# Kernel tuning notes

Hardware: AMD Instinct MI355X
Metric: run time of the kernel (lower is better)

## Reference

```python
import jax, jax.numpy as jnp
import numpy as np

B, S, H, D = 2, 2048, 16, 128
HID = H * D
ROPE_BASE = 10000.0


def _rope_tables(seq_len, dim, dtype):
    inv_freq = 1.0 / (ROPE_BASE ** (jnp.arange(0, dim, 2, dtype=jnp.float32) / dim))
    t = jnp.arange(seq_len, dtype=jnp.float32)
    freqs = jnp.einsum('s,d->sd', t, inv_freq)          # [S, D/2]
    emb = jnp.concatenate([freqs, freqs], axis=-1)       # [S, D]
    return jnp.cos(emb).astype(dtype), jnp.sin(emb).astype(dtype)


def _rotate_half(x):
    x1, x2 = jnp.split(x, 2, axis=-1)
    return jnp.concatenate([-x2, x1], axis=-1)


def _apply_rope(x, cos, sin, position_ids):
    # x: [B,H,S,D]; cos/sin: [S_emb, D]; position_ids: [B,S] or [1,S]
    c = cos[position_ids][:, None, :, :]  # [B,1,S,D]
    s = sin[position_ids][:, None, :, :]
    return x * c + _rotate_half(x) * s


def setup_inputs() -> dict:
    key = jax.random.key(0)
    ks = jax.random.split(key, 9)
    hidden_states = jax.random.normal(ks[0], (B, S, HID), jnp.float32) * 0.02
    Wq = jax.random.normal(ks[1], (HID, HID), jnp.float32) * 0.02
    Wk = jax.random.normal(ks[2], (HID, HID), jnp.float32) * 0.02
    Wv = jax.random.normal(ks[3], (HID, HID), jnp.float32) * 0.02
    Wo = jax.random.normal(ks[4], (HID, HID), jnp.float32) * 0.02
    # binary mask marking summary tokens
    sum_mask = jax.random.randint(ks[5], (B, S), 0, 2).astype(jnp.float32)
    # row-stochastic-ish averaging matrix over tokens (KV compression weights)
    raw = jax.random.uniform(ks[6], (B, S, S), jnp.float32)
    sum_attn_mask = sum_mask[:, :, None] * raw / jnp.sum(raw, axis=-1, keepdims=True)
    # additive causal mask [B,1,S,S]
    causal = jnp.tril(jnp.ones((S, S), dtype=bool))
    attention_mask = jnp.where(causal, 0.0, -1e9).astype(jnp.float32)
    attention_mask = jnp.broadcast_to(attention_mask[None, None], (B, 1, S, S))
    position_ids = jnp.broadcast_to(jnp.arange(S, dtype=jnp.int32), (B, S))
    return {
        'hidden_states': hidden_states, 'sum_mask': sum_mask,
        'sum_attn_mask': sum_attn_mask, 'attention_mask': attention_mask,
        'position_ids': position_ids, 'Wq': Wq, 'Wk': Wk, 'Wv': Wv, 'Wo': Wo,
    }


def reference(hidden_states, sum_mask, sum_attn_mask, attention_mask,
              position_ids, Wq, Wk, Wv, Wo):
    dtype = hidden_states.dtype
    # projections (F.linear: x @ W^T), then [B,H,S,D]
    def proj(W):
        return (hidden_states @ W.T).reshape(B, S, H, D).transpose(0, 2, 1, 3)
    q, k, v = proj(Wq), proj(Wk), proj(Wv)

    kv_seq_len = S
    cos, sin = _rope_tables(kv_seq_len, D, dtype)
    q = _apply_rope(q, cos, sin, position_ids)

    # KV compression: weighted token averaging injected at summary positions
    k_avg = jnp.einsum('bqk,bhkd->bhqd', sum_attn_mask, k)
    v_avg = jnp.einsum('bqk,bhkd->bhqd', sum_attn_mask, v)
    no_sum = (1.0 - sum_mask)[:, None, :, None]  # [B,1,S,1]
    k = no_sum * k + k_avg
    v = no_sum * v + v_avg

    key_pos = jnp.arange(kv_seq_len, dtype=jnp.int32)[None, :]  # [1,S]
    k = _apply_rope(k, cos, sin, key_pos)

    scale = 1.0 / np.sqrt(D)
    attn = jnp.einsum('bhqd,bhkd->bhqk', q, k) * scale
    attn = attn + attention_mask
    attn = jnp.maximum(attn, jnp.finfo(attn.dtype).min)
    attn = jax.nn.softmax(attn.astype(jnp.float32), axis=-1).astype(dtype)
    out = jnp.einsum('bhqk,bhkd->bhqd', attn, v)            # [B,H,S,D]
    out = out.transpose(0, 2, 1, 3).reshape(B, S, HID)
    return out @ Wo.T
```

## Files before the change

### kernel.cpp

```cpp
#include <hip/hip_runtime.h>
#include <cstdint>
#include <cstddef>

#define B_   2
#define S_   2048
#define H_   16
#define D_   128
#define HID_ 2048

typedef __bf16 bf16;
typedef unsigned short u16;
typedef bf16 bf16x4 __attribute__((ext_vector_type(4)));
typedef bf16 bf16x8 __attribute__((ext_vector_type(8)));
typedef u16  u16x8  __attribute__((ext_vector_type(8)));
typedef float f32x4 __attribute__((ext_vector_type(4)));

__device__ unsigned g_work;

__device__ __forceinline__ f32x4 mfma16(bf16x8 a, bf16x8 b, f32x4 c){
  return __builtin_amdgcn_mfma_f32_16x16x32_bf16(a, b, c, 0, 0, 0);
}

__device__ __forceinline__ void gload_lds16(const void* g, void* l){
  __builtin_amdgcn_global_load_lds((const __attribute__((address_space(1))) void*)g,
                                   (__attribute__((address_space(3))) void*)l, 16, 0, 0);
}

__device__ __forceinline__ void bar_lgkm(){
  asm volatile("s_waitcnt lgkmcnt(0)" ::: "memory");
  __builtin_amdgcn_s_barrier();
}
__device__ __forceinline__ void bar_full(){
  asm volatile("s_waitcnt vmcnt(0) lgkmcnt(0)" ::: "memory");
  __builtin_amdgcn_s_barrier();
}

__global__ void k_tables(float* __restrict__ cosT, float* __restrict__ sinT){
  if (blockIdx.x == 0 && threadIdx.x == 0) g_work = 0u;
  int id = blockIdx.x*256 + threadIdx.x;
  int p = id >> 6, i = id & 63;
  double f = (double)p * pow(10000.0, -(double)i/64.0);
  cosT[id] = (float)cos(f);
  sinT[id] = (float)sin(f);
}

__global__ void k_cvt_all(const float* __restrict__ a0, bf16* __restrict__ o0,
                          const float* __restrict__ a1, bf16* __restrict__ o1,
                          const float* __restrict__ w0, bf16* __restrict__ q0,
                          const float* __restrict__ w1, bf16* __restrict__ q1,
                          const float* __restrict__ w2, bf16* __restrict__ q2,
                          const float* __restrict__ w3, bf16* __restrict__ q3){
  const float* src; bf16* dst; int n4;
  switch (blockIdx.y){
    case 0: src = a0; dst = o0; n4 = 2097152; break;
    case 1: src = a1; dst = o1; n4 = 2097152; break;
    case 2: src = w0; dst = q0; n4 = 1048576; break;
    case 3: src = w1; dst = q1; n4 = 1048576; break;
    case 4: src = w2; dst = q2; n4 = 1048576; break;
    default: src = w3; dst = q3; n4 = 1048576; break;
  }
  int i = blockIdx.x*256 + threadIdx.x;
  if (i >= n4) return;
  f32x4 v = *reinterpret_cast<const f32x4*>(src + (size_t)i*4);
  bf16x4 o;
  o[0]=(bf16)v[0]; o[1]=(bf16)v[1]; o[2]=(bf16)v[2]; o[3]=(bf16)v[3];
  *reinterpret_cast<bf16x4*>(dst + (size_t)i*4) = o;
}

__global__ __launch_bounds__(256) void k_transpose_cvt(const float* __restrict__ in, bf16* __restrict__ out){
  __shared__ bf16 t[64][72];
  const int tid = threadIdx.x;
  const int b = blockIdx.z, j0 = blockIdx.x*64, s0 = blockIdx.y*64;
  #pragma unroll
  for (int u0 = 0; u0 < 4; ++u0){
    int u = u0*256 + tid;
    int r = u >> 4, c4 = (u & 15)*4;
    f32x4 v = *reinterpret_cast<const f32x4*>(in + ((size_t)b*S_ + s0 + r)*HID_ + j0 + c4);
    bf16x4 o; o[0]=(bf16)v[0]; o[1]=(bf16)v[1]; o[2]=(bf16)v[2]; o[3]=(bf16)v[3];
    *reinterpret_cast<bf16x4*>(&t[r][c4]) = o;
  }
  __syncthreads();
  #pragma unroll
  for (int u0 = 0; u0 < 4; ++u0){
    int u = u0*256 + tid;
    int r = u >> 4, c4 = (u & 15)*4;
    bf16x4 o;
    o[0] = t[c4+0][r]; o[1] = t[c4+1][r]; o[2] = t[c4+2][r]; o[3] = t[c4+3][r];
    *reinterpret_cast<bf16x4*>(out + ((size_t)b*HID_ + j0 + r)*S_ + s0 + c4) = o;
  }
}

template<int EPI>
__global__ __launch_bounds__(256) void k_gemm_nt(
    const bf16* __restrict__ A, const bf16* __restrict__ Bm, void* __restrict__ Cv,
    int Kd, size_t sAz, size_t sBz, size_t sCz, int N,
    const float* __restrict__ mask, const float* __restrict__ hid)
{
  const int tid = threadIdx.x;
  const int wid = tid >> 6, lane = tid & 63;
  const int g = lane >> 4, li = lane & 15;
  const int z = blockIdx.z;
  const int m0 = blockIdx.y*128, n0 = blockIdx.x*128;
  const int wm = wid >> 1, wn = wid & 1;
  const bf16* Ab = A + (size_t)z*sAz;
  const bf16* Bb = Bm + (size_t)z*sBz;

  __shared__ bf16 lA[128*64];
  __shared__ bf16 lB[128*64];

  f32x4 acc[4][4];
  #pragma unroll
  for (int i=0;i<4;++i)
    #pragma unroll
    for (int j=0;j<4;++j)
      acc[i][j] = {0.f,0.f,0.f,0.f};

  for (int k0 = 0; k0 < Kd; k0 += 64){
    #pragma unroll
    for (int j=0;j<4;++j){
      int ci = j*256 + tid;
      int r = ci >> 3, cb = ci & 7;
      gload_lds16(Ab + (size_t)(m0 + r)*Kd + k0 + cb*8, (char*)lA + (j*256 + wid*64)*16);
      gload_lds16(Bb + (size_t)(n0 + r)*Kd + k0 + cb*8, (char*)lB + (j*256 + wid*64)*16);
    }
    __syncthreads();
    #pragma unroll
    for (int kk=0;kk<2;++kk){
      bf16x8 af[4], bfm[4];
      #pragma unroll
      for (int i=0;i<4;++i){
        af[i]  = *reinterpret_cast<const bf16x8*>(&lA[(wm*64 + i*16 + li)*64 + kk*32 + g*8]);
        bfm[i] = *reinterpret_cast<const bf16x8*>(&lB[(wn*64 + i*16 + li)*64 + kk*32 + g*8]);
      }
      #pragma unroll
      for (int i=0;i<4;++i)
        #pragma unroll
        for (int j=0;j<4;++j)
          acc[i][j] = mfma16(af[i], bfm[j], acc[i][j]);
    }
    __syncthreads();
  }

  #pragma unroll
  for (int i=0;i<4;++i){
    #pragma unroll
    for (int j=0;j<4;++j){
      #pragma unroll
      for (int v=0;v<4;++v){
        int row = m0 + wm*64 + i*16 + g*4 + v;
        int col = n0 + wn*64 + j*16 + li;
        float x = acc[i][j][v];
        if (EPI == 1){
          x += (1.f - mask[z*S_ + row]) * hid[((size_t)z*S_ + row)*HID_ + col];
          ((bf16*)Cv)[(size_t)z*sCz + (size_t)row*N + col] = (bf16)x;
        } else if (EPI == 0){
          ((bf16*)Cv)[(size_t)row*N + col] = (bf16)x;
        } else if (EPI == 2){
          ((float*)Cv)[(size_t)row*N + col] = x;
        } else {
          if (n0 < 2048) ((bf16*)Cv)[(size_t)row*2048 + col] = (bf16)x;
          else ((bf16*)(void*)hid)[(size_t)row*2048 + col - 2048] = (bf16)x;
        }
      }
    }
  }
}

__global__ void k_rope(bf16* __restrict__ X, const float* __restrict__ cosT,
                       const float* __restrict__ sinT, const int* __restrict__ pos){
  int id = blockIdx.x*256 + threadIdx.x;
  int d4 = (id & 15)*4;
  int h  = (id >> 4) & 15;
  int s  = (id >> 8) & 2047;
  int b  = id >> 19;
  int p = pos ? pos[b*S_ + s] : s;
  size_t base = (((size_t)b*S_ + s)*H_ + h)*D_ + d4;
  f32x4 c  = *reinterpret_cast<const f32x4*>(cosT + (size_t)p*64 + d4);
  f32x4 sn = *reinterpret_cast<const f32x4*>(sinT + (size_t)p*64 + d4);
  bf16x4 x1 = *reinterpret_cast<bf16x4*>(X + base);
  bf16x4 x2 = *reinterpret_cast<bf16x4*>(X + base + 64);
  bf16x4 o1, o2;
  #pragma unroll
  for (int i=0;i<4;++i){
    float a = (float)x1[i], bb = (float)x2[i];
    o1[i] = (bf16)(a*c[i] - bb*sn[i]);
    o2[i] = (bf16)(bb*c[i] + a*sn[i]);
  }
  *reinterpret_cast<bf16x4*>(X + base) = o1;
  *reinterpret_cast<bf16x4*>(X + base + 64) = o2;
}

__global__ __launch_bounds__(256,2) void k_flash(const bf16* __restrict__ Q, const bf16* __restrict__ K,
                                                 const bf16* __restrict__ V, bf16* __restrict__ O,
                                                 float* __restrict__ OP, float* __restrict__ ML)
{
  const int tid = threadIdx.x;
  const int wid = tid >> 6, lane = tid & 63;
  const int g = lane >> 4, li = lane & 15;

  __shared__ bf16 Klds[2][64*128];
  __shared__ char VtB[128*128];
  __shared__ bf16 Plds[4][32*72];
  __shared__ int s_item;

  const int dc0 = tid & 15, kvp0 = tid >> 4;
  const int kvp1 = kvp0 + 16;

  for (;;) {
    if (tid == 0) s_item = (int)atomicAdd(&g_work, 1u);
    __syncthreads();
    const int w = s_item;
    if (w >= 672) return;

    int qx, bh, part, t0, t1;
    if (w < 96)       { qx = 10 - (w >> 5);  bh = w & 31;  part = -1; t0 = 0; t1 = 2*qx + 2; }
    else if (w < 416) { int u = w - 96;  qx = 15 - (u >> 6); int r = u & 63; bh = r >> 1; part = r & 1;
                        int nt = 2*qx + 2, mid = nt >> 1; t0 = part ? mid : 0; t1 = part ? nt : mid; }
    else              { int u = w - 416; qx = 7 - (u >> 5);  bh = u & 31;  part = -1; t0 = 0; t1 = 2*qx + 2; }

    const int qb = qx * 128;
    const size_t headoff = ((size_t)(bh >> 4)*S_*H_ + (bh & 15))*D_;
    const bf16* Kh = K + headoff;
    const u16*  Vh = (const u16*)(V + headoff);

    bf16x8 qf[2][4];
    #pragma unroll
    for (int rb=0;rb<2;++rb){
      const bf16* Qp = Q + headoff + (size_t)(qb + wid*32 + rb*16 + li)*H_*D_;
      #pragma unroll
      for (int kc=0;kc<4;++kc)
        qf[rb][kc] = *reinterpret_cast<const bf16x8*>(Qp + kc*32 + g*8);
    }

    float mrun[2][4], lrun[2][4];
    f32x4 acc[2][8];
    #pragma unroll
    for (int rb=0;rb<2;++rb){
      #pragma unroll
      for (int v=0;v<4;++v){ mrun[rb][v] = -1e30f; lrun[rb][v] = 0.f; }
      #pragma unroll
      for (int fn=0;fn<8;++fn) acc[rb][fn] = {0.f,0.f,0.f,0.f};
    }

    u16x8 vp[4];
    auto stageK = [&](int buf, int t){
      #pragma unroll
      for (int j=0;j<4;++j){
        int ci = j*256 + tid;
        int r = ci >> 4, cb = ci & 15;
        const char* src = (const char*)(Kh + (size_t)(t*64 + r)*H_*D_) + ((cb ^ (r & 7)) * 16);
        gload_lds16(src, (char*)Klds[buf] + (j*256 + wid*64)*16);
      }
    };
    auto loadV = [&](int t){
      const u16* s0p = Vh + (size_t)(t*64 + kvp0*2)*H_*D_ + dc0*8;
      const u16* s1p = Vh + (size_t)(t*64 + kvp1*2)*H_*D_ + dc0*8;
      vp[0] = *reinterpret_cast<const u16x8*>(s0p);
      vp[1] = *reinterpret_cast<const u16x8*>(s0p + H_*D_);
      vp[2] = *reinterpret_cast<const u16x8*>(s1p);
      vp[3] = *reinterpret_cast<const u16x8*>(s1p + H_*D_);
    };
    auto writeVtB = [&](){
      #pragma unroll
      for (int j=0;j<2;++j){
        int kvp = j ? kvp1 : kvp0;
        #pragma unroll
        for (int e=0;e<8;++e){
          int r = dc0*8 + e;
          int swz = (r ^ (r >> 3)) & 7;
          int addr = r*128 + (((kvp >> 2) ^ swz) << 4) + ((kvp << 2) & 12);
          *reinterpret_cast<uint32_t*>(VtB + addr) =
              (uint32_t)vp[j*2+0][e] | ((uint32_t)vp[j*2+1][e] << 16);
        }
      }
    };

    stageK(0, t0);
    loadV(t0);
    writeVtB();
    bar_full();

    int cur = 0;
    for (int t=t0; t<t1; ++t){
      const bool more = (t+1 < t1);
      if (more){ stageK(cur^1, t+1); loadV(t+1); }

      f32x4 sc[2][4];
      #pragma unroll
      for (int fc=0;fc<4;++fc){
        int r = fc*16 + li;
        bf16x8 kf[4];
        #pragma unroll
        for (int kc=0;kc<4;++kc)
          kf[kc] = *reinterpret_cast<const bf16x8*>((const char*)Klds[cur] + r*256 + (((4*kc + g) ^ (r & 7))*16));
        __builtin_amdgcn_s_setprio(1);
        #pragma unroll
        for (int rb=0;rb<2;++rb){
          f32x4 s = {0.f,0.f,0.f,0.f};
          #pragma unroll
          for (int kc=0;kc<4;++kc)
            s = mfma16(qf[rb][kc], kf[kc], s);
          sc[rb][fc] = s;
        }
        __builtin_amdgcn_s_setprio(0);
      }

      const float scale = 0.08838834764831845f;
      const int c0 = t*64;
      if (t >= 2*qx){
        #pragma unroll
        for (int rb=0;rb<2;++rb){
          const int rowg = qb + wid*32 + rb*16 + g*4;
          #pragma unroll
          for (int fc=0;fc<4;++fc){
            int col = c0 + fc*16 + li;
            #pragma unroll
            for (int v=0;v<4;++v){
              float s = sc[rb][fc][v] * scale;
              sc[rb][fc][v] = (col > rowg + v) ? -1e30f : s;
            }
          }
        }
      } else {
        #pragma unroll
        for (int rb=0;rb<2;++rb)
          #pragma unroll
          for (int fc=0;fc<4;++fc)
            #pragma unroll
            for (int v=0;v<4;++v)
              sc[rb][fc][v] *= scale;
      }

      #pragma unroll
      for (int rb=0;rb<2;++rb){
        float tm[4];
        #pragma unroll
        for (int v=0;v<4;++v){
          float m2 = fmaxf(fmaxf(sc[rb][0][v], sc[rb][1][v]), fmaxf(sc[rb][2][v], sc[rb][3][v]));
          m2 = fmaxf(m2, __shfl_xor(m2, 1));
          m2 = fmaxf(m2, __shfl_xor(m2, 2));
          m2 = fmaxf(m2, __shfl_xor(m2, 4));
          m2 = fmaxf(m2, __shfl_xor(m2, 8));
          tm[v] = m2;
        }
        bool need = false;
        #pragma unroll
        for (int v=0;v<4;++v) need = need || (tm[v] > mrun[rb][v] + 8.f);
        if (__any(need)){
          float al[4];
          #pragma unroll
          for (int v=0;v<4;++v){
            float mnew = fmaxf(mrun[rb][v], tm[v]);
            al[v] = __expf(mrun[rb][v] - mnew);
            mrun[rb][v] = mnew;
            lrun[rb][v] *= al[v];
          }
          #pragma unroll
          for (int fn=0;fn<8;++fn)
            #pragma unroll
            for (int v=0;v<4;++v) acc[rb][fn][v] *= al[v];
        }
        float rs[4] = {0.f,0.f,0.f,0.f};
        #pragma unroll
        for (int fc=0;fc<4;++fc){
          #pragma unroll
          for (int v=0;v<4;++v){
            float p = __expf(sc[rb][fc][v] - mrun[rb][v]);
            rs[v] += p;
            Plds[wid][(rb*16 + g*4 + v)*72 + fc*16 + li] = (bf16)p;
          }
        }
        #pragma unroll
        for (int v=0;v<4;++v){
          float r = rs[v];
          r += __shfl_xor(r, 1); r += __shfl_xor(r, 2);
          r += __shfl_xor(r, 4); r += __shfl_xor(r, 8);
          lrun[rb][v] += r;
        }
      }

      bf16x8 pa[2][2];
      #pragma unroll
      for (int rb=0;rb<2;++rb)
        #pragma unroll
        for (int kc=0;kc<2;++kc)
          pa[rb][kc] = *reinterpret_cast<const bf16x8*>(&Plds[wid][(rb*16 + li)*72 + kc*32 + g*8]);
      #pragma unroll
      for (int fn=0;fn<8;++fn){
        int r = fn*16 + li;
        int swz = (r ^ (r >> 3)) & 7;
        bf16x8 bv[2];
        #pragma unroll
        for (int kc=0;kc<2;++kc)
          bv[kc] = *reinterpret_cast<const bf16x8*>(VtB + r*128 + (((kc*4 + g) ^ swz) << 4));
        __builtin_amdgcn_s_setprio(1);
        #pragma unroll
        for (int rb=0;rb<2;++rb)
          #pragma unroll
          for (int kc=0;kc<2;++kc)
            acc[rb][fn] = mfma16(pa[rb][kc], bv[kc], acc[rb][fn]);
        __builtin_amdgcn_s_setprio(0);
      }

      if (more){
        bar_lgkm();
        writeVtB();
      }
      bar_full();
      cur ^= 1;
    }

    if (part < 0){
      #pragma unroll
      for (int rb=0;rb<2;++rb){
        #pragma unroll
        for (int v=0;v<4;++v){
          float inv = 1.f / lrun[rb][v];
          int row = qb + wid*32 + rb*16 + g*4 + v;
          bf16* dst = O + headoff + (size_t)row*H_*D_ + li;
          #pragma unroll
          for (int fn=0;fn<8;++fn)
            dst[fn*16] = (bf16)(acc[rb][fn][v] * inv);
        }
      }
    } else {
      const int sidx = (15 - qx)*64 + (bh << 1) + part;
      float* Od = OP + (size_t)sidx*128*128;
      #pragma unroll
      for (int rb=0;rb<2;++rb){
        #pragma unroll
        for (int v=0;v<4;++v){
          int rl = wid*32 + rb*16 + g*4 + v;
          #pragma unroll
          for (int fn=0;fn<8;++fn)
            Od[rl*128 + fn*16 + li] = acc[rb][fn][v];
          if (li == 0){
            ML[(size_t)sidx*256 + rl*2 + 0] = mrun[rb][v];
            ML[(size_t)sidx*256 + rl*2 + 1] = lrun[rb][v];
          }
        }
      }
    }
  }
}

__global__ __launch_bounds__(256) void k_merge(const float* __restrict__ OP, const float* __restrict__ ML,
                                               bf16* __restrict__ O){
  const int pair = blockIdx.x;
  const int qi = pair >> 5;
  const int qx = 15 - qi;
  const int bh = pair & 31;
  const int s0 = qi*64 + (bh << 1), s1 = s0 + 1;
  const int b = bh >> 4, h = bh & 15;
  const int qb = qx * 128;
  const int row = threadIdx.x >> 1;
  const int cseg = (threadIdx.x & 1) * 64;

  float m0 = ML[(size_t)s0*256 + row*2], l0 = ML[(size_t)s0*256 + row*2 + 1];
  float m1 = ML[(size_t)s1*256 + row*2], l1 = ML[(size_t)s1*256 + row*2 + 1];
  float m = fmaxf(m0, m1);
  float e0 = __expf(m0 - m), e1 = __expf(m1 - m);
  float inv = 1.f / (l0*e0 + l1*e1);
  const float* O0 = OP + ((size_t)s0*128 + row)*128 + cseg;
  const float* O1 = OP + ((size_t)s1*128 + row)*128 + cseg;
  bf16* dst = O + (((size_t)b*S_ + qb + row)*H_ + h)*D_ + cseg;
  #pragma unroll
  for (int c=0; c<64; c+=4){
    f32x4 a = *reinterpret_cast<const f32x4*>(O0 + c);
    f32x4 bb = *reinterpret_cast<const f32x4*>(O1 + c);
    bf16x4 o;
    #pragma unroll
    for (int i=0;i<4;++i) o[i] = (bf16)((a[i]*e0 + bb[i]*e1) * inv);
    *reinterpret_cast<bf16x4*>(dst + c) = o;
  }
}

extern "C" void kernel_launch(void* const* d_in, const int* in_sizes, int n_in,
                              void* d_out, int out_size, void* d_ws, size_t ws_size,
                              hipStream_t stream)
{
  (void)in_sizes; (void)n_in; (void)out_size; (void)ws_size;
  const float* hid   = (const float*)d_in[0];
  const float* smask = (const float*)d_in[1];
  const float* samat = (const float*)d_in[2];
  const int*   pos   = (const int*)d_in[4];
  const float* Wq = (const float*)d_in[5];
  const float* Wk = (const float*)d_in[6];
  const float* Wv = (const float*)d_in[7];
  const float* Wo = (const float*)d_in[8];
  float* out = (float*)d_out;
  char* ws = (char*)d_ws;

  const size_t SZ_TAB = (size_t)S_*64*4;
  const size_t SZ_BSH = (size_t)B_*S_*HID_*2;
  float* cosT = (float*)(ws);
  float* sinT = (float*)(ws + SZ_TAB);
  bf16* buf1 = (bf16*)(ws + 2*SZ_TAB);
  bf16* buf2 = (bf16*)(ws + 2*SZ_TAB + 1*SZ_BSH);
  bf16* buf3 = (bf16*)(ws + 2*SZ_TAB + 2*SZ_BSH);
  bf16* buf4 = (bf16*)(ws + 2*SZ_TAB + 3*SZ_BSH);
  bf16* Wqb = (bf16*)(ws + 2*SZ_TAB + 4*SZ_BSH);
  bf16* Wkb = Wqb + (size_t)HID_*HID_;
  bf16* Wvb = Wkb + (size_t)HID_*HID_;
  bf16* Wob = Wvb + (size_t)HID_*HID_;
  float* OP = (float*)Wqb;
  float* ML = OP + (size_t)320*128*128;

  k_tables<<<512,256,0,stream>>>(cosT, sinT);
  k_cvt_all<<<dim3(8192,6),256,0,stream>>>(hid, buf1, samat, buf3,
                                           Wq, Wqb, Wk, Wkb, Wv, Wvb, Wo, Wob);
  k_transpose_cvt<<<dim3(32,32,2),256,0,stream>>>(hid, buf2);

  const size_t sBat = (size_t)S_*HID_;
  k_gemm_nt<1><<<dim3(16,16,2),256,0,stream>>>(buf3, buf2, buf4, 2048, sBat, sBat, sBat, 2048, smask, hid);
  k_gemm_nt<0><<<dim3(16,32,1),256,0,stream>>>(buf1, Wqb, buf3, 2048, 0,0,0, 2048, nullptr, nullptr);
  k_rope<<<4096,256,0,stream>>>(buf3, cosT, sinT, pos);
  k_gemm_nt<3><<<dim3(32,32,1),256,0,stream>>>(buf4, Wkb, buf2, 2048, 0,0,0, 2048, nullptr, (const float*)buf1);
  k_rope<<<4096,256,0,stream>>>(buf2, cosT, sinT, nullptr);
  k_flash<<<dim3(512),256,0,stream>>>(buf3, buf2, buf1, buf4, OP, ML);
  k_merge<<<dim3(160),256,0,stream>>>(OP, ML, buf4);
  k_gemm_nt<2><<<dim3(16,32,1),256,0,stream>>>(buf4, Wob, out, 2048, 0,0,0, 2048, nullptr, nullptr);
}
```

Measured before the change: 452.2 us.

## Add 256x256-tile double-buffered GEMM with swizzled LDS for fused K/V projection

Adds a new GEMM kernel with 512 threads, 256x256 output tiles, double-buffered LDS filled by direct global-to-LDS loads, an XOR-swizzled LDS layout, and MFMA bursts raised in priority with s_setprio. Only the fused K/V projection GEMM (N=4096) uses it, replacing the 128x128-tile kernel. The aim is more reuse per LDS load, fewer bank conflicts, and overlap of the next tile's loads with the current tile's MFMAs. In exchange it uses 128KB of LDS and 128 accumulator registers per thread, which limits occupancy, and the grid shrinks to 256 blocks.

```diff
diff --git a/kernel.cpp b/kernel.cpp
--- a/kernel.cpp
+++ b/kernel.cpp
@@ -148,6 +148,135 @@
       #pragma unroll
       for (int v=0;v<4;++v){
         int row = m0 + wm*64 + i*16 + g*4 + v;
+        int col = n0 + wn*64 + j*16 + li;
+        float x = acc[i][j][v];
+        if (EPI == 1){
+          x += (1.f - mask[z*S_ + row]) * hid[((size_t)z*S_ + row)*HID_ + col];
+          ((bf16*)Cv)[(size_t)z*sCz + (size_t)row*N + col] = (bf16)x;
+        } else if (EPI == 0){
+          ((bf16*)Cv)[(size_t)row*N + col] = (bf16)x;
+        } else if (EPI == 2){
+          ((float*)Cv)[(size_t)row*N + col] = x;
+        } else {
+          if (n0 < 2048) ((bf16*)Cv)[(size_t)row*2048 + col] = (bf16)x;
+          else ((bf16*)(void*)hid)[(size_t)row*2048 + col - 2048] = (bf16)x;
+        }
+      }
+    }
+  }
+}
+
+template<int EPI>
+__global__ __launch_bounds__(512,2) void k_gemm256(
+    const bf16* __restrict__ A, const bf16* __restrict__ Bm, void* __restrict__ Cv,
+    int Kd, size_t sAz, size_t sBz, size_t sCz, int N,
+    const float* __restrict__ mask, const float* __restrict__ hid)
+{
+  const int tid = threadIdx.x;
+  const int wid = tid >> 6, lane = tid & 63;
+  const int g = lane >> 4, li = lane & 15;
+  const int wm = wid >> 2, wn = wid & 3;
+  const int z = blockIdx.z;
+  const int m0 = blockIdx.y*256, n0 = blockIdx.x*256;
+  const bf16* Ab = A + (size_t)z*sAz + (size_t)m0*Kd;
+  const bf16* Bb = Bm + (size_t)z*sBz + (size_t)n0*Kd;
+
+  __shared__ bf16 lA[2][256*64];
+  __shared__ bf16 lB[2][256*64];
+
+  const int rr0 = tid >> 3, cc = tid & 7;
+  const int rr1 = rr0 + 64;
+  const int cx0 = cc ^ (rr0 & 7);
+  const int cx1 = cc ^ (rr1 & 7);
+
+  f32x4 acc[8][4];
+  #pragma unroll
+  for (int i=0;i<8;++i)
+    #pragma unroll
+    for (int j=0;j<4;++j) acc[i][j] = {0.f,0.f,0.f,0.f};
+
+  auto stage = [&](int buf, int kt, int matsel, int half){
+    const bf16* s = matsel ? Bb : Ab;
+    char* dbase = (char*)(matsel ? lB[buf] : lA[buf]) + half*16384;
+    gload_lds16(s + (size_t)(half*128 + rr0)*Kd + kt*64 + cx0*8, dbase + (wid*64)*16);
+    gload_lds16(s + (size_t)(half*128 + rr1)*Kd + kt*64 + cx1*8, dbase + (512 + wid*64)*16);
+  };
+  auto rdA = [&](int buf, int i, int kh){
+    int row = wm*128 + i*16 + li;
+    return *reinterpret_cast<const bf16x8*>((const char*)lA[buf] + row*128 + (((kh*4 + g) ^ (row & 7))*16));
+  };
+  auto rdB = [&](int buf, int j, int kh){
+    int row = wn*64 + j*16 + li;
+    return *reinterpret_cast<const bf16x8*>((const char*)lB[buf] + row*128 + (((kh*4 + g) ^ (row & 7))*16));
+  };
+
+  const int NT = Kd >> 6;
+  stage(0,0,0,0); stage(0,0,0,1); stage(0,0,1,0); stage(0,0,1,1);
+  __syncthreads();
+
+  int cur = 0;
+  for (int kt = 0; kt < NT; ++kt){
+    const bool more = (kt+1 < NT);
+    bf16x8 af[4], bfr[4];
+
+    if (more){
+      stage(cur^1, kt+1, 0, 0); stage(cur^1, kt+1, 0, 1);
+      stage(cur^1, kt+1, 1, 0); stage(cur^1, kt+1, 1, 1);
+    }
+    #pragma unroll
+    for (int i=0;i<4;++i) af[i] = rdA(cur, i, 0);
+    #pragma unroll
+    for (int j=0;j<4;++j) bfr[j] = rdB(cur, j, 0);
+    __builtin_amdgcn_s_setprio(1);
+    #pragma unroll
+    for (int i=0;i<4;++i)
+      #pragma unroll
+      for (int j=0;j<4;++j) acc[i][j] = mfma16(af[i], bfr[j], acc[i][j]);
+    __builtin_amdgcn_s_setprio(0);
+    __builtin_amdgcn_s_barrier();
+
+    #pragma unroll
+    for (int i=0;i<4;++i) af[i] = rdA(cur, i+4, 0);
+    __builtin_amdgcn_s_setprio(1);
+    #pragma unroll
+    for (int i=0;i<4;++i)
+      #pragma unroll
+      for (int j=0;j<4;++j) acc[i+4][j] = mfma16(af[i], bfr[j], acc[i+4][j]);
+    __builtin_amdgcn_s_setprio(0);
+    __builtin_amdgcn_s_barrier();
+
+    #pragma unroll
+    for (int i=0;i<4;++i) af[i] = rdA(cur, i, 1);
+    #pragma unroll
+    for (int j=0;j<4;++j) bfr[j] = rdB(cur, j, 1);
+    __builtin_amdgcn_s_setprio(1);
+    #pragma unroll
+    for (int i=0;i<4;++i)
+      #pragma unroll
+      for (int j=0;j<4;++j) acc[i][j] = mfma16(af[i], bfr[j], acc[i][j]);
+    __builtin_amdgcn_s_setprio(0);
+    __builtin_amdgcn_s_barrier();
+
+    #pragma unroll
+    for (int i=0;i<4;++i) af[i] = rdA(cur, i+4, 1);
+    __builtin_amdgcn_s_setprio(1);
+    #pragma unroll
+    for (int i=0;i<4;++i)
+      #pragma unroll
+      for (int j=0;j<4;++j) acc[i+4][j] = mfma16(af[i], bfr[j], acc[i+4][j]);
+    __builtin_amdgcn_s_setprio(0);
+
+    __syncthreads();
+    cur ^= 1;
+  }
+
+  #pragma unroll
+  for (int i=0;i<8;++i){
+    #pragma unroll
+    for (int j=0;j<4;++j){
+      #pragma unroll
+      for (int v=0;v<4;++v){
+        int row = m0 + wm*128 + i*16 + g*4 + v;
         int col = n0 + wn*64 + j*16 + li;
         float x = acc[i][j][v];
         if (EPI == 1){
@@ -515,7 +644,7 @@
   k_gemm_nt<1><<<dim3(16,16,2),256,0,stream>>>(buf3, buf2, buf4, 2048, sBat, sBat, sBat, 2048, smask, hid);
   k_gemm_nt<0><<<dim3(16,32,1),256,0,stream>>>(buf1, Wqb, buf3, 2048, 0,0,0, 2048, nullptr, nullptr);
   k_rope<<<4096,256,0,stream>>>(buf3, cosT, sinT, pos);
-  k_gemm_nt<3><<<dim3(32,32,1),256,0,stream>>>(buf4, Wkb, buf2, 2048, 0,0,0, 2048, nullptr, (const float*)buf1);
+  k_gemm256<3><<<dim3(16,16,1),512,0,stream>>>(buf4, Wkb, buf2, 2048, 0,0,0, 2048, nullptr, (const float*)buf1);
   k_rope<<<4096,256,0,stream>>>(buf2, cosT, sinT, nullptr);
   k_flash<<<dim3(512),256,0,stream>>>(buf3, buf2, buf1, buf4, OP, ML);
   k_merge<<<dim3(160),256,0,stream>>>(OP, ML, buf4);
```

New measurement: 427.3 us. -5.5%, faster.

## Replace GEMM with double-buffered 256-row tile kernel using swizzled LDS

Applied to the files above, without the earlier changes.

Replaces the single-buffered 128x128 GEMM with a 512-thread kernel that computes 256xBN tiles. It double-buffers global-to-LDS loads split into half-K stages, interleaves the next tile's loads with MFMA work, and guards stages with vmcnt waits and barriers. LDS rows are XOR-swizzled to avoid bank conflicts, and s_setprio wraps the MFMA blocks. The aim is to hide memory latency and raise data reuse, at the cost of more registers (launch bounds 512,2) and fewer blocks per GEMM.

```diff
diff --git a/kernel.cpp b/kernel.cpp
--- a/kernel.cpp
+++ b/kernel.cpp
@@ -24,6 +24,13 @@
 __device__ __forceinline__ void gload_lds16(const void* g, void* l){
   __builtin_amdgcn_global_load_lds((const __attribute__((address_space(1))) void*)g,
                                    (__attribute__((address_space(3))) void*)l, 16, 0, 0);
+}
+
+template<int N>
+__device__ __forceinline__ void wait_vm(){
+  if constexpr (N == 0) asm volatile("s_waitcnt vmcnt(0)" ::: "memory");
+  else if constexpr (N == 3) asm volatile("s_waitcnt vmcnt(3)" ::: "memory");
+  else asm volatile("s_waitcnt vmcnt(4)" ::: "memory");
 }
 
 __device__ __forceinline__ void bar_lgkm(){
@@ -90,65 +97,135 @@
   }
 }
 
-template<int EPI>
-__global__ __launch_bounds__(256) void k_gemm_nt(
+template<int EPI, int BN>
+__global__ __launch_bounds__(512,2) void k_gemm2(
     const bf16* __restrict__ A, const bf16* __restrict__ Bm, void* __restrict__ Cv,
     int Kd, size_t sAz, size_t sBz, size_t sCz, int N,
     const float* __restrict__ mask, const float* __restrict__ hid)
 {
+  constexpr int NW = (BN == 256) ? 4 : 3;
+  constexpr int MI = (BN == 256) ? 8 : 4;
+  constexpr int MH = MI/2;
   const int tid = threadIdx.x;
   const int wid = tid >> 6, lane = tid & 63;
   const int g = lane >> 4, li = lane & 15;
+  const int wm = (BN == 256) ? (wid >> 2) : (wid >> 1);
+  const int wn = (BN == 256) ? (wid & 3)  : (wid & 1);
+  const int mOff = wm * ((BN == 256) ? 128 : 64);
+  const int nOff = wn * 64;
   const int z = blockIdx.z;
-  const int m0 = blockIdx.y*128, n0 = blockIdx.x*128;
-  const int wm = wid >> 1, wn = wid & 1;
-  const bf16* Ab = A + (size_t)z*sAz;
-  const bf16* Bb = Bm + (size_t)z*sBz;
-
-  __shared__ bf16 lA[128*64];
-  __shared__ bf16 lB[128*64];
-
-  f32x4 acc[4][4];
+  const int m0 = blockIdx.y*256, n0 = blockIdx.x*BN;
+  const bf16* Ab = A + (size_t)z*sAz + (size_t)m0*Kd;
+  const bf16* Bb = Bm + (size_t)z*sBz + (size_t)n0*Kd;
+
+  __shared__ bf16 lA[2][2][256*32];
+  __shared__ bf16 lB[2][2][BN*32];
+
+  const int rq = tid >> 2, cq = tid & 3;
+  const int csw = cq ^ ((rq >> 1) & 3);
+
+  f32x4 acc[MI][4];
   #pragma unroll
-  for (int i=0;i<4;++i)
-    #pragma unroll
-    for (int j=0;j<4;++j)
-      acc[i][j] = {0.f,0.f,0.f,0.f};
-
-  for (int k0 = 0; k0 < Kd; k0 += 64){
+  for (int i=0;i<MI;++i)
+    #pragma unroll
+    for (int j=0;j<4;++j) acc[i][j] = {0.f,0.f,0.f,0.f};
+
+  auto stA = [&](int buf, int kt, int kh){
+    const bf16* s = Ab + (size_t)rq*Kd + kt*64 + kh*32 + csw*8;
+    char* d = (char*)lA[buf][kh];
+    gload_lds16(s, d + wid*1024);
+    gload_lds16(s + (size_t)128*Kd, d + 8192 + wid*1024);
+  };
+  auto stB = [&](int buf, int kt, int kh){
+    char* d = (char*)lB[buf][kh];
+    const bf16* s = Bb + (size_t)rq*Kd + kt*64 + kh*32 + csw*8;
+    if constexpr (BN == 256){
+      gload_lds16(s, d + wid*1024);
+      gload_lds16(s + (size_t)128*Kd, d + 8192 + wid*1024);
+    } else {
+      gload_lds16(s, d + wid*1024);
+    }
+  };
+  auto rdA = [&](int buf, int kh, int i){
+    int row = mOff + i*16 + li;
+    int c = g ^ ((row >> 1) & 3);
+    return *reinterpret_cast<const bf16x8*>((const char*)lA[buf][kh] + row*64 + c*16);
+  };
+  auto rdB = [&](int buf, int kh, int j){
+    int row = nOff + j*16 + li;
+    int c = g ^ ((row >> 1) & 3);
+    return *reinterpret_cast<const bf16x8*>((const char*)lB[buf][kh] + row*64 + c*16);
+  };
+
+  const int NT = Kd >> 6;
+  stA(0,0,0); stB(0,0,0); stA(0,0,1); stB(0,0,1);
+
+  int cur = 0;
+  for (int kt = 0; kt < NT; ++kt){
+    const bool more = (kt+1 < NT);
+    bf16x8 af[MH], bfr[4];
+
+    wait_vm<NW>();
+    __builtin_amdgcn_s_barrier();
+
+    if (more) stA(cur^1, kt+1, 0);
+    #pragma unroll
+    for (int j=0;j<4;++j) bfr[j] = rdB(cur, 0, j);
+    #pragma unroll
+    for (int i=0;i<MH;++i) af[i] = rdA(cur, 0, i);
+    __builtin_amdgcn_s_setprio(1);
+    #pragma unroll
+    for (int i=0;i<MH;++i)
+      #pragma unroll
+      for (int j=0;j<4;++j) acc[i][j] = mfma16(af[i], bfr[j], acc[i][j]);
+    __builtin_amdgcn_s_setprio(0);
+
+    if (more) stB(cur^1, kt+1, 0);
+    #pragma unroll
+    for (int i=0;i<MH;++i) af[i] = rdA(cur, 0, MH+i);
+    __builtin_amdgcn_s_setprio(1);
+    #pragma unroll
+    for (int i=0;i<MH;++i)
+      #pragma unroll
+      for (int j=0;j<4;++j) acc[MH+i][j] = mfma16(af[i], bfr[j], acc[MH+i][j]);
+    __builtin_amdgcn_s_setprio(0);
+
+    if (more) wait_vm<NW>(); else wait_vm<0>();
+    __builtin_amdgcn_s_barrier();
+
+    if (more) stA(cur^1, kt+1, 1);
+    #pragma unroll
+    for (int j=0;j<4;++j) bfr[j] = rdB(cur, 1, j);
+    #pragma unroll
+    for (int i=0;i<MH;++i) af[i] = rdA(cur, 1, i);
+    __builtin_amdgcn_s_setprio(1);
+    #pragma unroll
+    for (int i=0;i<MH;++i)
+      #pragma unroll
+      for (int j=0;j<4;++j) acc[i][j] = mfma16(af[i], bfr[j], acc[i][j]);
+    __builtin_amdgcn_s_setprio(0);
+
+    if (more) stB(cur^1, kt+1, 1);
+    #pragma unroll
+    for (int i=0;i<MH;++i) af[i] = rdA(cur, 1, MH+i);
+    __builtin_amdgcn_s_setprio(1);
+    #pragma unroll
+    for (int i=0;i<MH;++i)
+      #pragma unroll
+      for (int j=0;j<4;++j) acc[MH+i][j] = mfma16(af[i], bfr[j], acc[MH+i][j]);
+    __builtin_amdgcn_s_setprio(0);
+
+    cur ^= 1;
+  }
+
+  #pragma unroll
+  for (int i=0;i<MI;++i){
     #pragma unroll
     for (int j=0;j<4;++j){
-      int ci = j*256 + tid;
-      int r = ci >> 3, cb = ci & 7;
-      gload_lds16(Ab + (size_t)(m0 + r)*Kd + k0 + cb*8, (char*)lA + (j*256 + wid*64)*16);
-      gload_lds16(Bb + (size_t)(n0 + r)*Kd + k0 + cb*8, (char*)lB + (j*256 + wid*64)*16);
-    }
-    __syncthreads();
-    #pragma unroll
-    for (int kk=0;kk<2;++kk){
-      bf16x8 af[4], bfm[4];
-      #pragma unroll
-      for (int i=0;i<4;++i){
-        af[i]  = *reinterpret_cast<const bf16x8*>(&lA[(wm*64 + i*16 + li)*64 + kk*32 + g*8]);
-        bfm[i] = *reinterpret_cast<const bf16x8*>(&lB[(wn*64 + i*16 + li)*64 + kk*32 + g*8]);
-      }
-      #pragma unroll
-      for (int i=0;i<4;++i)
-        #pragma unroll
-        for (int j=0;j<4;++j)
-          acc[i][j] = mfma16(af[i], bfm[j], acc[i][j]);
-    }
-    __syncthreads();
-  }
-
-  #pragma unroll
-  for (int i=0;i<4;++i){
-    #pragma unroll
-    for (int j=0;j<4;++j){
       #pragma unroll
       for (int v=0;v<4;++v){
-        int row = m0 + wm*64 + i*16 + g*4 + v;
-        int col = n0 + wn*64 + j*16 + li;
+        int row = m0 + mOff + i*16 + g*4 + v;
+        int col = n0 + nOff + j*16 + li;
         float x = acc[i][j][v];
         if (EPI == 1){
           x += (1.f - mask[z*S_ + row]) * hid[((size_t)z*S_ + row)*HID_ + col];
@@ -512,12 +589,12 @@
   k_transpose_cvt<<<dim3(32,32,2),256,0,stream>>>(hid, buf2);
 
   const size_t sBat = (size_t)S_*HID_;
-  k_gemm_nt<1><<<dim3(16,16,2),256,0,stream>>>(buf3, buf2, buf4, 2048, sBat, sBat, sBat, 2048, smask, hid);
-  k_gemm_nt<0><<<dim3(16,32,1),256,0,stream>>>(buf1, Wqb, buf3, 2048, 0,0,0, 2048, nullptr, nullptr);
+  k_gemm2<1,128><<<dim3(16,8,2),512,0,stream>>>(buf3, buf2, buf4, 2048, sBat, sBat, sBat, 2048, smask, hid);
+  k_gemm2<0,128><<<dim3(16,16,1),512,0,stream>>>(buf1, Wqb, buf3, 2048, 0,0,0, 2048, nullptr, nullptr);
   k_rope<<<4096,256,0,stream>>>(buf3, cosT, sinT, pos);
-  k_gemm_nt<3><<<dim3(32,32,1),256,0,stream>>>(buf4, Wkb, buf2, 2048, 0,0,0, 2048, nullptr, (const float*)buf1);
+  k_gemm2<3,256><<<dim3(16,16,1),512,0,stream>>>(buf4, Wkb, buf2, 2048, 0,0,0, 4096, nullptr, (const float*)buf1);
   k_rope<<<4096,256,0,stream>>>(buf2, cosT, sinT, nullptr);
   k_flash<<<dim3(512),256,0,stream>>>(buf3, buf2, buf1, buf4, OP, ML);
   k_merge<<<dim3(160),256,0,stream>>>(OP, ML, buf4);
-  k_gemm_nt<2><<<dim3(16,32,1),256,0,stream>>>(buf4, Wob, out, 2048, 0,0,0, 2048, nullptr, nullptr);
-}
+  k_gemm2<2,128><<<dim3(16,16,1),512,0,stream>>>(buf4, Wob, out, 2048, 0,0,0, 2048, nullptr, nullptr);
+}
```

After: 450.8 us. About the same (-0.3%).
